# Kernel optimization log

Measured on AMD Instinct MI355X. Metric: run time of the kernel, lower is better.

Reference implementation:

```python
import jax, jax.numpy as jnp
import numpy as np

B, S, H, NH, NF = 128, 1024, 768, 8, 8
FUSED = 3 * H + NF  # 2312


def _lin(k, o, i):
    return jax.random.normal(k, (o, i), jnp.float32) * (1.0 / np.sqrt(i))


def setup_inputs() -> dict:
    key = jax.random.key(0)
    ks = jax.random.split(key, 20)
    last_hidden = jax.random.normal(ks[0], (B, S, H), jnp.float32)
    arousal_feats = jax.random.normal(ks[1], (B, NF), jnp.float32)
    sep1 = jax.random.randint(ks[2], (B,), 2, 800)
    sep2 = jnp.minimum(sep1 + jax.random.randint(ks[3], (B,), 2, 200), S - 1)
    return {
        "last_hidden": last_hidden,
        "arousal_feats": arousal_feats,
        "sep1": sep1,
        "sep2": sep2,
        "in_proj_w": _lin(ks[4], 3 * H, H),
        "in_proj_b": jnp.zeros((3 * H,), jnp.float32),
        "out_w": _lin(ks[5], H, H),
        "out_b": jnp.zeros((H,), jnp.float32),
        "ln_g": jnp.ones((NF,), jnp.float32),
        "ln_b": jnp.zeros((NF,), jnp.float32),
        "va_w1": _lin(ks[6], 512, FUSED),
        "va_b1": jnp.zeros((512,), jnp.float32),
        "va_w2": _lin(ks[7], 128, 512),
        "va_b2": jnp.zeros((128,), jnp.float32),
        "va_w3": _lin(ks[8], 2, 128),
        "va_b3": jnp.zeros((2,), jnp.float32),
        "pol_w": _lin(ks[9], 3, FUSED),
        "pol_b": jnp.zeros((3,), jnp.float32),
        "aro_w": _lin(ks[10], 3, FUSED),
        "aro_b": jnp.zeros((3,), jnp.float32),
    }


def reference(last_hidden, arousal_feats, sep1, sep2, in_proj_w, in_proj_b,
              out_w, out_b, ln_g, ln_b, va_w1, va_b1, va_w2, va_b2,
              va_w3, va_b3, pol_w, pol_b, aro_w, aro_b):
    b, s, h = last_hidden.shape
    nh, dh = NH, h // NH
    pos = jnp.arange(s)[None, :]  # [1,S]
    # ragged boundaries -> masks (honors s1>1 / s2>s1+1 fallbacks to CLS token)
    text_mask = jnp.where((sep1 > 1)[:, None], (pos >= 1) & (pos < sep1[:, None]), pos == 0)
    asp_mask = jnp.where((sep2 > sep1 + 1)[:, None], (pos > sep1[:, None]) & (pos < sep2[:, None]), pos == 0)
    amf = asp_mask.astype(last_hidden.dtype)
    asp_query = (last_hidden * amf[..., None]).sum(1) / amf.sum(1)[:, None]  # [B,H]
    # MultiheadAttention with a single query per sample, keys/values masked to text span
    wq, wk, wv = jnp.split(in_proj_w, 3, axis=0)
    bq, bk, bv = jnp.split(in_proj_b, 3)
    q = (asp_query @ wq.T + bq).reshape(b, nh, dh)
    k = (last_hidden @ wk.T + bk).reshape(b, s, nh, dh)
    v = (last_hidden @ wv.T + bv).reshape(b, s, nh, dh)
    scale = 1.0 / np.sqrt(dh)
    scores = jnp.einsum('bhd,bshd->bhs', q, k) * scale
    scores = jnp.where(text_mask[:, None, :], scores, -jnp.inf)
    attn = jax.nn.softmax(scores, axis=-1)
    ctx = jnp.einsum('bhs,bshd->bhd', attn, v).reshape(b, h)
    cross = ctx @ out_w.T + out_b  # [B,H]
    # ArousalFeatureNorm ~ LayerNorm over feature dim
    mu = arousal_feats.mean(-1, keepdims=True)
    var = arousal_feats.var(-1, keepdims=True)
    aro_n = (arousal_feats - mu) / jnp.sqrt(var + 1e-5) * ln_g + ln_b
    fused = jnp.concatenate([last_hidden[:, 0], cross, asp_query, aro_n], axis=-1)
    hdn = jax.nn.gelu(fused @ va_w1.T + va_b1, approximate=False)
    hdn = jax.nn.gelu(hdn @ va_w2.T + va_b2, approximate=False)
    va = hdn @ va_w3.T + va_b3
    pol = fused @ pol_w.T + pol_b
    aro = fused @ aro_w.T + aro_b
    return (va, pol, aro)
```

## Files before the change

kernel.cpp:

```cpp
#include <hip/hip_runtime.h>
#include <hip/hip_bf16.h>
#include <math.h>

#define B 128
#define S 1024
#define H 768
#define NH 8
#define DH 96
#define FUSED 2312
#define KCHUNK 128
#define NOUT 544
#define MD 800
#define NZ_NOCTX 13
#define NZ_CTX 5
#define NZTOT 18
#define ASL 8
#define NSL 16
#define FCH 16
#define SCALE 0.10206207261596575f
#define GELU_C 0.70710678118654752f

#define MTILES (17 * 25)
#define HTILES (NZ_NOCTX * 4 * 17)

__device__ __forceinline__ float dot4(float4 a, float4 b) {
    return a.x * b.x + a.y * b.y + a.z * b.z + a.w * b.w;
}
__device__ __forceinline__ float gelu(float x) {
    return 0.5f * x * (1.0f + erff(x * GELU_C));
}

__device__ __forceinline__ const float* wrow_sel(int n, const float* va_w1,
                                                 const float* pol_w,
                                                 const float* aro_w,
                                                 bool& valid) {
    valid = true;
    if (n < 512) return va_w1 + (size_t)n * FUSED;
    if (n < 515) return pol_w + (size_t)(n - 512) * FUSED;
    if (n < 518) return aro_w + (size_t)(n - 515) * FUSED;
    valid = false;
    return va_w1;
}

__global__ __launch_bounds__(256) void k1_aspq_m(
        const float* __restrict__ lh,
        const int* __restrict__ sep1,
        const int* __restrict__ sep2,
        const float* __restrict__ va_w1,
        const float* __restrict__ pol_w,
        const float* __restrict__ aro_w,
        const float* __restrict__ out_w,
        const float* __restrict__ out_b,
        float* __restrict__ aspp,
        float* __restrict__ Mbuf) {
    int bid = blockIdx.x, t = threadIdx.x;
    if (bid < B * ASL) {
        if (t >= 192) return;
        int b = bid >> 3, z = bid & 7;
        int s1 = sep1[b], s2 = sep2[b];
        int lo, hi;
        if (s2 > s1 + 1) { lo = s1 + 1; hi = s2; } else { lo = 0; hi = 1; }
        const float* base = lh + ((size_t)b * S) * H + 4 * t;
        float4 a = {0.f, 0.f, 0.f, 0.f};
        for (int s = lo + z; s < hi; s += ASL) {
            float4 r = *(const float4*)(base + (size_t)s * H);
            a.x += r.x; a.y += r.y; a.z += r.z; a.w += r.w;
        }
        *(float4*)(aspp + (size_t)z * (B * H) + b * H + 4 * t) = a;
        return;
    }
    int j = bid - B * ASL;
    int n0 = (j / 25) * 32, d0 = (j % 25) * 32;
    __shared__ float As[32][33];
    __shared__ float Ws[32][33];
    int tx = t & 31, ty = t >> 5;
    int lr = t >> 3, lc = (t & 7) * 4;
    float acc[4] = {0.f, 0.f, 0.f, 0.f};
    for (int k0 = 0; k0 < H; k0 += 32) {
        {
            int n = n0 + lr;
            bool valid;
            const float* wr = wrow_sel(n, va_w1, pol_w, aro_w, valid);
            float4 a = {0.f, 0.f, 0.f, 0.f};
            if (valid) a = *(const float4*)(wr + H + k0 + lc);
            As[lr][lc] = a.x; As[lr][lc + 1] = a.y;
            As[lr][lc + 2] = a.z; As[lr][lc + 3] = a.w;
        }
        {
            int c = k0 + lr;
            float4 w;
            if (d0 < H) {
                w = *(const float4*)(out_w + (size_t)c * H + d0 + lc);
            } else {
                w.x = (lc == 0) ? out_b[c] : 0.f;
                w.y = 0.f; w.z = 0.f; w.w = 0.f;
            }
            Ws[lc][lr] = w.x; Ws[lc + 1][lr] = w.y;
            Ws[lc + 2][lr] = w.z; Ws[lc + 3][lr] = w.w;
        }
        __syncthreads();
#pragma unroll
        for (int kk = 0; kk < 32; ++kk) {
            float wv = Ws[tx][kk];
#pragma unroll
            for (int i = 0; i < 4; ++i)
                acc[i] += As[ty + 8 * i][kk] * wv;
        }
        __syncthreads();
    }
#pragma unroll
    for (int i = 0; i < 4; ++i)
        Mbuf[(size_t)(n0 + ty + 8 * i) * MD + d0 + tx] = acc[i];
}

__global__ void qu_kernel(const float* __restrict__ aspp,
                          const int* __restrict__ sep1,
                          const int* __restrict__ sep2,
                          const float* __restrict__ wq,
                          const float* __restrict__ bq,
                          const float* __restrict__ wk,
                          float* __restrict__ aspq,
                          float* __restrict__ U) {
    int h = blockIdx.x, b = blockIdx.y, t = threadIdx.x;
    int s1 = sep1[b], s2 = sep2[b];
    int lo, hi;
    if (s2 > s1 + 1) { lo = s1 + 1; hi = s2; } else { lo = 0; hi = 1; }
    float inv = 1.0f / (float)(hi - lo);
    __shared__ float aq[H];
    __shared__ float qh[DH];
    for (int c = t; c < H; c += 256) {
        float a = 0.f;
#pragma unroll
        for (int z = 0; z < ASL; ++z)
            a += aspp[(size_t)z * (B * H) + b * H + c];
        a *= inv;
        aq[c] = a;
        if (h == 0) aspq[b * H + c] = a;
    }
    __syncthreads();
    int wave = t >> 6, lane = t & 63;
#pragma unroll
    for (int i = 0; i < 24; ++i) {
        int d = wave * 24 + i;
        const float* wrow = wq + (size_t)(h * DH + d) * H;
        float a = 0.f;
#pragma unroll
        for (int j = 0; j < H / 64; ++j) a += wrow[lane + 64 * j] * aq[lane + 64 * j];
        for (int off = 32; off; off >>= 1) a += __shfl_xor(a, off);
        if (lane == 0) qh[d] = a + bq[h * DH + d];
    }
    __syncthreads();
    if (t < 192) {
        float4 u = {0.f, 0.f, 0.f, 0.f};
        for (int d = 0; d < DH; ++d) {
            float qd = qh[d];
            float4 w = *(const float4*)(wk + (size_t)(h * DH + d) * H + 4 * t);
            u.x += qd * w.x; u.y += qd * w.y;
            u.z += qd * w.z; u.w += qd * w.w;
        }
        *(float4*)(U + ((size_t)b * NH + h) * H + 4 * t) = u;
    }
}

__global__ __launch_bounds__(512) void k3_flash_hdn1(
        const float* __restrict__ lhg,
        const float* __restrict__ U,
        const int* __restrict__ sep1,
        const float* __restrict__ aspq,
        const float* __restrict__ aro_f,
        const float* __restrict__ ln_g,
        const float* __restrict__ ln_b,
        const float* __restrict__ va_w1,
        const float* __restrict__ pol_w,
        const float* __restrict__ aro_w,
        float* __restrict__ Op,
        float* __restrict__ mlb,
        float* __restrict__ hdn1p) {
    __shared__ float smem[FCH * H];
    int bid = blockIdx.x, t = threadIdx.x;

    if (bid < B * NSL) {
        int b = bid >> 4, z = bid & 15;
        int wave = t >> 6, lane = t & 63;
        int s1 = sep1[b];
        int tlo = (s1 > 1) ? 1 : 0;
        int thi = (s1 > 1) ? s1 : 1;
        int span = thi - tlo;
        int nrows = (span > z) ? ((span - z - 1) / NSL + 1) : 0;
        float (*lhs)[H] = (float(*)[H])smem;

        const float4* Uh = (const float4*)(U + ((size_t)b * NH + wave) * H);
        float4 u0 = Uh[lane], u1 = Uh[lane + 64], u2 = Uh[lane + 128];
        float4 O0 = {0.f, 0.f, 0.f, 0.f}, O1 = O0, O2 = O0;
        float m = -1e30f, l = 0.f;
        int rid = t >> 5, cid = t & 31;

        for (int j0 = 0; j0 < nrows; j0 += FCH) {
            int nv = min(FCH, nrows - j0);
            if (rid < nv) {
                int sg = tlo + z + NSL * (j0 + rid);
                const float4* row = (const float4*)(lhg + ((size_t)b * S + sg) * H);
                float4* dst = (float4*)lhs[rid];
#pragma unroll
                for (int k = 0; k < 6; ++k) dst[cid + 32 * k] = row[cid + 32 * k];
            }
            __syncthreads();
            for (int r = 0; r < nv; ++r) {
                const float4* xr = (const float4*)lhs[r];
                float4 x0 = xr[lane], x1 = xr[lane + 64], x2 = xr[lane + 128];
                float s = dot4(u0, x0) + dot4(u1, x1) + dot4(u2, x2);
                for (int off = 32; off; off >>= 1) s += __shfl_xor(s, off);
                s *= SCALE;
                if (s <= m) {
                    float p = __expf(s - m);
                    l += p;
                    O0.x += p * x0.x; O0.y += p * x0.y; O0.z += p * x0.z; O0.w += p * x0.w;
                    O1.x += p * x1.x; O1.y += p * x1.y; O1.z += p * x1.z; O1.w += p * x1.w;
                    O2.x += p * x2.x; O2.y += p * x2.y; O2.z += p * x2.z; O2.w += p * x2.w;
                } else {
                    float c = __expf(m - s);
                    m = s;
                    l = l * c + 1.0f;
                    O0.x = O0.x * c + x0.x; O0.y = O0.y * c + x0.y;
                    O0.z = O0.z * c + x0.z; O0.w = O0.w * c + x0.w;
                    O1.x = O1.x * c + x1.x; O1.y = O1.y * c + x1.y;
                    O1.z = O1.z * c + x1.z; O1.w = O1.w * c + x1.w;
                    O2.x = O2.x * c + x2.x; O2.y = O2.y * c + x2.y;
                    O2.z = O2.z * c + x2.z; O2.w = O2.w * c + x2.w;
                }
            }
            __syncthreads();
        }
        float4* Ob = (float4*)(Op + (((size_t)z * B + b) * NH + wave) * H);
        Ob[lane] = O0; Ob[lane + 64] = O1; Ob[lane + 128] = O2;
        if (lane == 0) {
            float* ml = mlb + ((size_t)z * B + b) * NH * 2;
            ml[2 * wave]     = m;
            ml[2 * wave + 1] = l;
        }
        return;
    }

    int j = bid - B * NSL;
    int z13 = j / 68, rem = j % 68;
    int z = (z13 < 6) ? z13 : z13 + 6;
    int m0 = (rem / 17) * 32, n0 = (rem % 17) * 32;
    int kbase = z * KCHUNK;
    float (*As)[33] = (float(*)[33])smem;
    float (*Ws)[33] = (float(*)[33])(smem + 32 * 33);
    int tx = t & 31, ty = t >> 5;
    int lr = t >> 3, lc = (t & 7) * 4;
    float acc[4] = {0.f, 0.f, 0.f, 0.f};
    bool active = (t < 256);
    for (int k0 = kbase; k0 < kbase + KCHUNK; k0 += 32) {
        if (active) {
            int bb = m0 + lr;
            int k = k0 + lc;
            float4 a;
            if (k < 768) {
                a = *(const float4*)(lhg + (size_t)bb * S * H + k);
            } else if (k < 2304) {
                a = *(const float4*)(aspq + (size_t)bb * H + (k - 1536));
            } else if (k < FUSED) {
                const float* af = aro_f + bb * 8;
                float mu = 0.f;
#pragma unroll
                for (int jj = 0; jj < 8; ++jj) mu += af[jj];
                mu *= 0.125f;
                float var = 0.f;
#pragma unroll
                for (int jj = 0; jj < 8; ++jj) { float d = af[jj] - mu; var += d * d; }
                var *= 0.125f;
                float rs = rsqrtf(var + 1e-5f);
                int c = k - 2304;
                a.x = (af[c]     - mu) * rs * ln_g[c]     + ln_b[c];
                a.y = (af[c + 1] - mu) * rs * ln_g[c + 1] + ln_b[c + 1];
                a.z = (af[c + 2] - mu) * rs * ln_g[c + 2] + ln_b[c + 2];
                a.w = (af[c + 3] - mu) * rs * ln_g[c + 3] + ln_b[c + 3];
            } else {
                a = {0.f, 0.f, 0.f, 0.f};
            }
            As[lr][lc] = a.x; As[lr][lc + 1] = a.y;
            As[lr][lc + 2] = a.z; As[lr][lc + 3] = a.w;
            int n = n0 + lr;
            int kk = min(k0 + lc, FUSED - 4);
            bool valid;
            const float* wr = wrow_sel(n, va_w1, pol_w, aro_w, valid);
            float4 w = {0.f, 0.f, 0.f, 0.f};
            if (valid) w = *(const float4*)(wr + kk);
            Ws[lr][lc] = w.x; Ws[lr][lc + 1] = w.y;
            Ws[lr][lc + 2] = w.z; Ws[lr][lc + 3] = w.w;
        }
        __syncthreads();
        if (active) {
#pragma unroll
            for (int kk = 0; kk < 32; ++kk) {
                float wv = Ws[tx][kk];
#pragma unroll
                for (int i = 0; i < 4; ++i)
                    acc[i] += As[ty + 8 * i][kk] * wv;
            }
        }
        __syncthreads();
    }
    if (active) {
        int n = n0 + tx;
#pragma unroll
        for (int i = 0; i < 4; ++i) {
            int mm = m0 + ty + 8 * i;
            hdn1p[(size_t)z13 * (B * NOUT) + (size_t)mm * NOUT + n] = acc[i];
        }
    }
}

__global__ void mergectx_kernel(const float* __restrict__ Op,
                                const float* __restrict__ mlb,
                                const float* __restrict__ wv,
                                const float* __restrict__ bv,
                                float* __restrict__ ctx) {
    int h = blockIdx.x, b = blockIdx.y, t = threadIdx.x;
    float M = -1e30f;
#pragma unroll
    for (int z = 0; z < NSL; ++z)
        M = fmaxf(M, mlb[(((size_t)z * B + b) * NH + h) * 2]);
    float wz[NSL], L = 0.f;
#pragma unroll
    for (int z = 0; z < NSL; ++z) {
        const float* ml = mlb + (((size_t)z * B + b) * NH + h) * 2;
        float e = __expf(ml[0] - M);
        wz[z] = e;
        L += e * ml[1];
    }
    float Li = 1.0f / L;
    __shared__ float wsum[H];
    for (int c = t; c < H; c += 256) {
        float a = 0.f;
#pragma unroll
        for (int z = 0; z < NSL; ++z)
            a += wz[z] * Op[(((size_t)z * B + b) * NH + h) * H + c];
        wsum[c] = a * Li;
    }
    __syncthreads();
    int wave = t >> 6, lane = t & 63;
#pragma unroll
    for (int i = 0; i < 24; ++i) {
        int d = wave * 24 + i;
        const float* wrow = wv + (size_t)(h * DH + d) * H;
        float a = 0.f;
#pragma unroll
        for (int j = 0; j < H / 64; ++j) a += wrow[lane + 64 * j] * wsum[lane + 64 * j];
        for (int off = 32; off; off >>= 1) a += __shfl_xor(a, off);
        if (lane == 0) ctx[b * H + h * DH + d] = a + bv[h * DH + d];
    }
}

__global__ __launch_bounds__(256) void k5_hdn1ctx(
        const float* __restrict__ ctx,
        const float* __restrict__ Mbuf,
        float* __restrict__ hdn1p) {
    int z = blockIdx.z;
    int n0 = blockIdx.x * 32, m0 = blockIdx.y * 32;
    int kbase = z * 160;
    __shared__ float As[32][33];
    __shared__ float Ws[32][33];
    int t = threadIdx.x;
    int tx = t & 31, ty = t >> 5;
    int lr = t >> 3, lc = (t & 7) * 4;
    float acc[4] = {0.f, 0.f, 0.f, 0.f};
    for (int k0 = kbase; k0 < kbase + 160; k0 += 32) {
        {
            int bb = m0 + lr;
            int k = k0 + lc;
            float4 a;
            if (k < 768)      a = *(const float4*)(ctx + (size_t)bb * H + k);
            else if (k == 768) a = {1.f, 0.f, 0.f, 0.f};
            else              a = {0.f, 0.f, 0.f, 0.f};
            As[lr][lc] = a.x; As[lr][lc + 1] = a.y;
            As[lr][lc + 2] = a.z; As[lr][lc + 3] = a.w;
        }
        {
            float4 w = *(const float4*)(Mbuf + (size_t)(n0 + lr) * MD + k0 + lc);
            Ws[lr][lc] = w.x; Ws[lr][lc + 1] = w.y;
            Ws[lr][lc + 2] = w.z; Ws[lr][lc + 3] = w.w;
        }
        __syncthreads();
#pragma unroll
        for (int kk = 0; kk < 32; ++kk) {
            float wv = Ws[tx][kk];
#pragma unroll
            for (int i = 0; i < 4; ++i)
                acc[i] += As[ty + 8 * i][kk] * wv;
        }
        __syncthreads();
    }
    int n = n0 + tx;
#pragma unroll
    for (int i = 0; i < 4; ++i) {
        int mm = m0 + ty + 8 * i;
        hdn1p[(size_t)(NZ_NOCTX + z) * (B * NOUT) + (size_t)mm * NOUT + n] = acc[i];
    }
}

__global__ __launch_bounds__(512) void mlp2_kernel(
        const float* __restrict__ hdn1p,
        const float* __restrict__ va_b1,
        const float* __restrict__ va_w2,
        const float* __restrict__ va_b2,
        const float* __restrict__ va_w3,
        const float* __restrict__ va_b3,
        const float* __restrict__ pol_b,
        const float* __restrict__ aro_b,
        float* __restrict__ out) {
    int b = blockIdx.x, t = threadIdx.x;
    int wave = t >> 6, lane = t & 63;
    __shared__ float hsS[512];
    __shared__ float h2S[128];
    {
        float s = 0.f;
#pragma unroll
        for (int z = 0; z < NZTOT; ++z)
            s += hdn1p[(size_t)z * (B * NOUT) + (size_t)b * NOUT + t];
        hsS[t] = gelu(s + va_b1[t]);
    }
    if (t < 6) {
        float s = 0.f;
#pragma unroll
        for (int z = 0; z < NZTOT; ++z)
            s += hdn1p[(size_t)z * (B * NOUT) + (size_t)b * NOUT + 512 + t];
        if (t < 3) out[256 + b * 3 + t]       = s + pol_b[t];
        else       out[640 + b * 3 + (t - 3)] = s + aro_b[t - 3];
    }
    __syncthreads();
#pragma unroll
    for (int i = 0; i < 16; ++i) {
        int n = wave * 16 + i;
        float a = 0.f;
#pragma unroll
        for (int j = 0; j < 8; ++j) {
            int k = lane + 64 * j;
            a += hsS[k] * va_w2[(size_t)n * 512 + k];
        }
        for (int off = 32; off; off >>= 1) a += __shfl_xor(a, off);
        if (lane == 0) h2S[n] = gelu(a + va_b2[n]);
    }
    __syncthreads();
    if (wave < 2) {
        float a = h2S[lane] * va_w3[wave * 128 + lane]
                + h2S[lane + 64] * va_w3[wave * 128 + lane + 64];
        for (int off = 32; off; off >>= 1) a += __shfl_xor(a, off);
        if (lane == 0) out[b * 2 + wave] = a + va_b3[wave];
    }
}

extern "C" void kernel_launch(void* const* d_in, const int* in_sizes, int n_in,
                              void* d_out, int out_size, void* d_ws, size_t ws_size,
                              hipStream_t stream) {
    const float* lh    = (const float*)d_in[0];
    const float* aro_f = (const float*)d_in[1];
    const int*   sep1  = (const int*)d_in[2];
    const int*   sep2  = (const int*)d_in[3];
    const float* in_w  = (const float*)d_in[4];
    const float* in_b  = (const float*)d_in[5];
    const float* out_w = (const float*)d_in[6];
    const float* out_b = (const float*)d_in[7];
    const float* ln_g  = (const float*)d_in[8];
    const float* ln_b  = (const float*)d_in[9];
    const float* va_w1 = (const float*)d_in[10];
    const float* va_b1 = (const float*)d_in[11];
    const float* va_w2 = (const float*)d_in[12];
    const float* va_b2 = (const float*)d_in[13];
    const float* va_w3 = (const float*)d_in[14];
    const float* va_b3 = (const float*)d_in[15];
    const float* pol_w = (const float*)d_in[16];
    const float* pol_b = (const float*)d_in[17];
    const float* aro_w = (const float*)d_in[18];
    const float* aro_b = (const float*)d_in[19];
    float* out = (float*)d_out;

    float* ws = (float*)d_ws;
    float* aspp   = ws;
    float* aspq   = aspp + ASL * B * H;
    float* Ubuf   = aspq + B * H;
    float* Opb    = Ubuf + B * NH * H;
    float* mlbuf  = Opb + (size_t)NSL * B * NH * H;
    float* ctx    = mlbuf + NSL * B * NH * 2;
    float* Mbuf   = ctx + B * H;
    float* hdn1p  = Mbuf + NOUT * MD;

    const float* wq = in_w;
    const float* wk = in_w + H * H;
    const float* wv = in_w + 2 * H * H;
    const float* bq = in_b;
    const float* bv = in_b + 2 * H;

    k1_aspq_m<<<B * ASL + MTILES, 256, 0, stream>>>(
        lh, sep1, sep2, va_w1, pol_w, aro_w, out_w, out_b, aspp, Mbuf);
    qu_kernel<<<dim3(NH, B), 256, 0, stream>>>(aspp, sep1, sep2, wq, bq, wk,
                                               aspq, Ubuf);
    k3_flash_hdn1<<<B * NSL + HTILES, 512, 0, stream>>>(
        lh, Ubuf, sep1, aspq, aro_f, ln_g, ln_b,
        va_w1, pol_w, aro_w, Opb, mlbuf, hdn1p);
    mergectx_kernel<<<dim3(NH, B), 256, 0, stream>>>(Opb, mlbuf, wv, bv, ctx);
    k5_hdn1ctx<<<dim3(17, 4, NZ_CTX), 256, 0, stream>>>(ctx, Mbuf, hdn1p);
    mlp2_kernel<<<B, 512, 0, stream>>>(hdn1p, va_b1, va_w2, va_b2,
                                       va_w3, va_b3, pol_b, aro_b, out);
}
```

Before: 214.3 us.

## Fuse six kernel launches into one cooperative persistent kernel with grid syncs

```diff
diff --git a/kernel.cpp b/kernel.cpp
--- a/kernel.cpp
+++ b/kernel.cpp
@@ -1,6 +1,9 @@
 #include <hip/hip_runtime.h>
+#include <hip/hip_cooperative_groups.h>
 #include <hip/hip_bf16.h>
 #include <math.h>
+
+namespace cg = cooperative_groups;
 
 #define B 128
 #define S 1024
@@ -17,11 +20,16 @@
 #define ASL 8
 #define NSL 16
 #define FCH 16
+#define GRID 256
 #define SCALE 0.10206207261596575f
 #define GELU_C 0.70710678118654752f
 
-#define MTILES (17 * 25)
-#define HTILES (NZ_NOCTX * 4 * 17)
+#define AJOBS (B * ASL)
+#define MJOBS (17 * 25)
+#define H1JOBS (7 * 4 * 17)
+#define H3JOBS (6 * 4 * 17)
+#define P0JOBS (AJOBS + MJOBS + H1JOBS)
+#define P2JOBS (B * NSL + H3JOBS)
 
 __device__ __forceinline__ float dot4(float4 a, float4 b) {
     return a.x * b.x + a.y * b.y + a.z * b.z + a.w * b.w;
@@ -29,7 +37,6 @@
 __device__ __forceinline__ float gelu(float x) {
     return 0.5f * x * (1.0f + erff(x * GELU_C));
 }
-
 __device__ __forceinline__ const float* wrow_sel(int n, const float* va_w1,
                                                  const float* pol_w,
                                                  const float* aro_w,
@@ -41,6 +48,470 @@
     valid = false;
     return va_w1;
 }
+
+__global__ __launch_bounds__(512, 4) void mega_kernel(
+        const float* __restrict__ lh,
+        const float* __restrict__ aro_f,
+        const int* __restrict__ sep1,
+        const int* __restrict__ sep2,
+        const float* __restrict__ in_w,
+        const float* __restrict__ in_b,
+        const float* __restrict__ out_w,
+        const float* __restrict__ out_b,
+        const float* __restrict__ ln_g,
+        const float* __restrict__ ln_b,
+        const float* __restrict__ va_w1,
+        const float* __restrict__ va_b1,
+        const float* __restrict__ va_w2,
+        const float* __restrict__ va_b2,
+        const float* __restrict__ va_w3,
+        const float* __restrict__ va_b3,
+        const float* __restrict__ pol_w,
+        const float* __restrict__ pol_b,
+        const float* __restrict__ aro_w,
+        const float* __restrict__ aro_b,
+        float* __restrict__ ws,
+        float* __restrict__ out) {
+    cg::grid_group gridg = cg::this_grid();
+    __shared__ float smem[FCH * H];
+
+    float* aspp  = ws;
+    float* aspq  = aspp + ASL * B * H;
+    float* Ubuf  = aspq + B * H;
+    float* Opb   = Ubuf + B * NH * H;
+    float* mlbuf = Opb + (size_t)NSL * B * NH * H;
+    float* ctx   = mlbuf + NSL * B * NH * 2;
+    float* Mbuf  = ctx + B * H;
+    float* hdn1p = Mbuf + NOUT * MD;
+
+    const float* wq = in_w;
+    const float* wk = in_w + H * H;
+    const float* wv = in_w + 2 * H * H;
+    const float* bq = in_b;
+    const float* bv = in_b + 2 * H;
+
+    int t = threadIdx.x;
+    int wave = t >> 6, lane = t & 63;
+    int nblk = gridDim.x;
+
+    for (int j = blockIdx.x; j < P0JOBS; j += nblk) {
+        if (j < AJOBS) {
+            if (t < 192) {
+                int b = j >> 3, z = j & 7;
+                int s1 = sep1[b], s2 = sep2[b];
+                int lo, hi;
+                if (s2 > s1 + 1) { lo = s1 + 1; hi = s2; } else { lo = 0; hi = 1; }
+                const float* base = lh + ((size_t)b * S) * H + 4 * t;
+                float4 a = {0.f, 0.f, 0.f, 0.f};
+                for (int s = lo + z; s < hi; s += ASL) {
+                    float4 r = *(const float4*)(base + (size_t)s * H);
+                    a.x += r.x; a.y += r.y; a.z += r.z; a.w += r.w;
+                }
+                *(float4*)(aspp + (size_t)z * (B * H) + b * H + 4 * t) = a;
+            }
+            __syncthreads();
+            continue;
+        }
+        float (*As)[33] = (float(*)[33])smem;
+        float (*Ws)[33] = (float(*)[33])(smem + 32 * 33);
+        int tx = t & 31, ty = (t >> 5) & 7;
+        int lr = (t & 255) >> 3, lc = (t & 7) * 4;
+        bool active = (t < 256);
+        float acc[4] = {0.f, 0.f, 0.f, 0.f};
+        if (j < AJOBS + MJOBS) {
+            int jm = j - AJOBS;
+            int n0 = (jm / 25) * 32, d0 = (jm % 25) * 32;
+            for (int k0 = 0; k0 < H; k0 += 32) {
+                if (active) {
+                    int n = n0 + lr;
+                    bool valid;
+                    const float* wr = wrow_sel(n, va_w1, pol_w, aro_w, valid);
+                    float4 a = {0.f, 0.f, 0.f, 0.f};
+                    if (valid) a = *(const float4*)(wr + H + k0 + lc);
+                    As[lr][lc] = a.x; As[lr][lc + 1] = a.y;
+                    As[lr][lc + 2] = a.z; As[lr][lc + 3] = a.w;
+                    int c = k0 + lr;
+                    float4 w;
+                    if (d0 < H) {
+                        w = *(const float4*)(out_w + (size_t)c * H + d0 + lc);
+                    } else {
+                        w.x = (lc == 0) ? out_b[c] : 0.f;
+                        w.y = 0.f; w.z = 0.f; w.w = 0.f;
+                    }
+                    Ws[lc][lr] = w.x; Ws[lc + 1][lr] = w.y;
+                    Ws[lc + 2][lr] = w.z; Ws[lc + 3][lr] = w.w;
+                }
+                __syncthreads();
+                if (active) {
+#pragma unroll
+                    for (int kk = 0; kk < 32; ++kk) {
+                        float wv2 = Ws[tx][kk];
+#pragma unroll
+                        for (int i = 0; i < 4; ++i)
+                            acc[i] += As[ty + 8 * i][kk] * wv2;
+                    }
+                }
+                __syncthreads();
+            }
+            if (active) {
+#pragma unroll
+                for (int i = 0; i < 4; ++i)
+                    Mbuf[(size_t)(n0 + ty + 8 * i) * MD + d0 + tx] = acc[i];
+            }
+            continue;
+        }
+        int jh = j - AJOBS - MJOBS;
+        int z13 = jh / 68, rem = jh % 68;
+        int z    = (z13 < 6) ? z13 : 18;
+        int slot = (z13 < 6) ? z13 : 12;
+        int m0 = (rem / 17) * 32, n0 = (rem % 17) * 32;
+        int kbase = z * KCHUNK;
+        for (int k0 = kbase; k0 < kbase + KCHUNK; k0 += 32) {
+            if (active) {
+                int bb = m0 + lr;
+                int k = k0 + lc;
+                float4 a;
+                if (k < 768) {
+                    a = *(const float4*)(lh + (size_t)bb * S * H + k);
+                } else if (k < FUSED) {
+                    const float* af = aro_f + bb * 8;
+                    float mu = 0.f;
+#pragma unroll
+                    for (int jj = 0; jj < 8; ++jj) mu += af[jj];
+                    mu *= 0.125f;
+                    float var = 0.f;
+#pragma unroll
+                    for (int jj = 0; jj < 8; ++jj) { float d = af[jj] - mu; var += d * d; }
+                    var *= 0.125f;
+                    float rs = rsqrtf(var + 1e-5f);
+                    int c = k - 2304;
+                    a.x = (af[c]     - mu) * rs * ln_g[c]     + ln_b[c];
+                    a.y = (af[c + 1] - mu) * rs * ln_g[c + 1] + ln_b[c + 1];
+                    a.z = (af[c + 2] - mu) * rs * ln_g[c + 2] + ln_b[c + 2];
+                    a.w = (af[c + 3] - mu) * rs * ln_g[c + 3] + ln_b[c + 3];
+                } else {
+                    a = {0.f, 0.f, 0.f, 0.f};
+                }
+                As[lr][lc] = a.x; As[lr][lc + 1] = a.y;
+                As[lr][lc + 2] = a.z; As[lr][lc + 3] = a.w;
+                int n = n0 + lr;
+                int kk = min(k0 + lc, FUSED - 4);
+                bool valid;
+                const float* wr = wrow_sel(n, va_w1, pol_w, aro_w, valid);
+                float4 w = {0.f, 0.f, 0.f, 0.f};
+                if (valid) w = *(const float4*)(wr + kk);
+                Ws[lr][lc] = w.x; Ws[lr][lc + 1] = w.y;
+                Ws[lr][lc + 2] = w.z; Ws[lr][lc + 3] = w.w;
+            }
+            __syncthreads();
+            if (active) {
+#pragma unroll
+                for (int kk = 0; kk < 32; ++kk) {
+                    float wv2 = Ws[tx][kk];
+#pragma unroll
+                    for (int i = 0; i < 4; ++i)
+                        acc[i] += As[ty + 8 * i][kk] * wv2;
+                }
+            }
+            __syncthreads();
+        }
+        if (active) {
+            int n = n0 + tx;
+#pragma unroll
+            for (int i = 0; i < 4; ++i) {
+                int mm = m0 + ty + 8 * i;
+                hdn1p[(size_t)slot * (B * NOUT) + (size_t)mm * NOUT + n] = acc[i];
+            }
+        }
+    }
+    gridg.sync();
+
+    for (int j = blockIdx.x; j < B * NH; j += nblk) {
+        int b = j >> 3, h = j & 7;
+        float* aq = smem;
+        float* qh = smem + H;
+        int s1 = sep1[b], s2 = sep2[b];
+        int lo, hi;
+        if (s2 > s1 + 1) { lo = s1 + 1; hi = s2; } else { lo = 0; hi = 1; }
+        float inv = 1.0f / (float)(hi - lo);
+        for (int c = t; c < H; c += 512) {
+            float a = 0.f;
+#pragma unroll
+            for (int z = 0; z < ASL; ++z)
+                a += aspp[(size_t)z * (B * H) + b * H + c];
+            a *= inv;
+            aq[c] = a;
+            if (h == 0) aspq[b * H + c] = a;
+        }
+        __syncthreads();
+#pragma unroll
+        for (int i = 0; i < 12; ++i) {
+            int d = wave * 12 + i;
+            const float* wrow = wq + (size_t)(h * DH + d) * H;
+            float a = 0.f;
+#pragma unroll
+            for (int jj = 0; jj < H / 64; ++jj)
+                a += wrow[lane + 64 * jj] * aq[lane + 64 * jj];
+            for (int off = 32; off; off >>= 1) a += __shfl_xor(a, off);
+            if (lane == 0) qh[d] = a + bq[h * DH + d];
+        }
+        __syncthreads();
+        if (t < 192) {
+            float4 u = {0.f, 0.f, 0.f, 0.f};
+            for (int d = 0; d < DH; ++d) {
+                float qd = qh[d];
+                float4 w = *(const float4*)(wk + (size_t)(h * DH + d) * H + 4 * t);
+                u.x += qd * w.x; u.y += qd * w.y;
+                u.z += qd * w.z; u.w += qd * w.w;
+            }
+            *(float4*)(Ubuf + ((size_t)b * NH + h) * H + 4 * t) = u;
+        }
+        __syncthreads();
+    }
+    gridg.sync();
+
+    for (int j = blockIdx.x; j < P2JOBS; j += nblk) {
+        if (j < B * NSL) {
+            int b = j >> 4, z = j & 15;
+            int s1 = sep1[b];
+            int tlo = (s1 > 1) ? 1 : 0;
+            int thi = (s1 > 1) ? s1 : 1;
+            int span = thi - tlo;
+            int nrows = (span > z) ? ((span - z - 1) / NSL + 1) : 0;
+            float (*lhs)[H] = (float(*)[H])smem;
+
+            const float4* Uh = (const float4*)(Ubuf + ((size_t)b * NH + wave) * H);
+            float4 u0 = Uh[lane], u1 = Uh[lane + 64], u2 = Uh[lane + 128];
+            float4 O0 = {0.f, 0.f, 0.f, 0.f}, O1 = O0, O2 = O0;
+            float m = -1e30f, l = 0.f;
+            int rid = t >> 5, cid = t & 31;
+
+            for (int j0 = 0; j0 < nrows; j0 += FCH) {
+                int nv = min(FCH, nrows - j0);
+                if (rid < nv) {
+                    int sg = tlo + z + NSL * (j0 + rid);
+                    const float4* row = (const float4*)(lh + ((size_t)b * S + sg) * H);
+                    float4* dst = (float4*)lhs[rid];
+#pragma unroll
+                    for (int k = 0; k < 6; ++k) dst[cid + 32 * k] = row[cid + 32 * k];
+                }
+                __syncthreads();
+                for (int r = 0; r < nv; ++r) {
+                    const float4* xr = (const float4*)lhs[r];
+                    float4 x0 = xr[lane], x1 = xr[lane + 64], x2 = xr[lane + 128];
+                    float s = dot4(u0, x0) + dot4(u1, x1) + dot4(u2, x2);
+                    for (int off = 32; off; off >>= 1) s += __shfl_xor(s, off);
+                    s *= SCALE;
+                    if (s <= m) {
+                        float p = __expf(s - m);
+                        l += p;
+                        O0.x += p * x0.x; O0.y += p * x0.y; O0.z += p * x0.z; O0.w += p * x0.w;
+                        O1.x += p * x1.x; O1.y += p * x1.y; O1.z += p * x1.z; O1.w += p * x1.w;
+                        O2.x += p * x2.x; O2.y += p * x2.y; O2.z += p * x2.z; O2.w += p * x2.w;
+                    } else {
+                        float c = __expf(m - s);
+                        m = s;
+                        l = l * c + 1.0f;
+                        O0.x = O0.x * c + x0.x; O0.y = O0.y * c + x0.y;
+                        O0.z = O0.z * c + x0.z; O0.w = O0.w * c + x0.w;
+                        O1.x = O1.x * c + x1.x; O1.y = O1.y * c + x1.y;
+                        O1.z = O1.z * c + x1.z; O1.w = O1.w * c + x1.w;
+                        O2.x = O2.x * c + x2.x; O2.y = O2.y * c + x2.y;
+                        O2.z = O2.z * c + x2.z; O2.w = O2.w * c + x2.w;
+                    }
+                }
+                __syncthreads();
+            }
+            float4* Ob = (float4*)(Opb + (((size_t)z * B + b) * NH + wave) * H);
+            Ob[lane] = O0; Ob[lane + 64] = O1; Ob[lane + 128] = O2;
+            if (lane == 0) {
+                float* ml = mlbuf + ((size_t)z * B + b) * NH * 2;
+                ml[2 * wave]     = m;
+                ml[2 * wave + 1] = l;
+            }
+            __syncthreads();
+            continue;
+        }
+        int jh = j - B * NSL;
+        int zi = jh / 68, rem = jh % 68;
+        int z = zi + 12, slot = zi + 6;
+        int m0 = (rem / 17) * 32, n0 = (rem % 17) * 32;
+        int kbase = z * KCHUNK;
+        float (*As)[33] = (float(*)[33])smem;
+        float (*Ws)[33] = (float(*)[33])(smem + 32 * 33);
+        int tx = t & 31, ty = (t >> 5) & 7;
+        int lr = (t & 255) >> 3, lc = (t & 7) * 4;
+        float acc[4] = {0.f, 0.f, 0.f, 0.f};
+        bool active = (t < 256);
+        for (int k0 = kbase; k0 < kbase + KCHUNK; k0 += 32) {
+            if (active) {
+                int bb = m0 + lr;
+                int k = k0 + lc;
+                float4 a = *(const float4*)(aspq + (size_t)bb * H + (k - 1536));
+                As[lr][lc] = a.x; As[lr][lc + 1] = a.y;
+                As[lr][lc + 2] = a.z; As[lr][lc + 3] = a.w;
+                int n = n0 + lr;
+                bool valid;
+                const float* wr = wrow_sel(n, va_w1, pol_w, aro_w, valid);
+                float4 w = {0.f, 0.f, 0.f, 0.f};
+                if (valid) w = *(const float4*)(wr + k);
+                Ws[lr][lc] = w.x; Ws[lr][lc + 1] = w.y;
+                Ws[lr][lc + 2] = w.z; Ws[lr][lc + 3] = w.w;
+            }
+            __syncthreads();
+            if (active) {
+#pragma unroll
+                for (int kk = 0; kk < 32; ++kk) {
+                    float wv2 = Ws[tx][kk];
+#pragma unroll
+                    for (int i = 0; i < 4; ++i)
+                        acc[i] += As[ty + 8 * i][kk] * wv2;
+                }
+            }
+            __syncthreads();
+        }
+        if (active) {
+            int n = n0 + tx;
+#pragma unroll
+            for (int i = 0; i < 4; ++i) {
+                int mm = m0 + ty + 8 * i;
+                hdn1p[(size_t)slot * (B * NOUT) + (size_t)mm * NOUT + n] = acc[i];
+            }
+        }
+    }
+    gridg.sync();
+
+    for (int j = blockIdx.x; j < B * NH; j += nblk) {
+        int b = j >> 3, h = j & 7;
+        float* wsum = smem;
+        float M = -1e30f;
+#pragma unroll
+        for (int z = 0; z < NSL; ++z)
+            M = fmaxf(M, mlbuf[(((size_t)z * B + b) * NH + h) * 2]);
+        float wz[NSL], L = 0.f;
+#pragma unroll
+        for (int z = 0; z < NSL; ++z) {
+            const float* ml = mlbuf + (((size_t)z * B + b) * NH + h) * 2;
+            float e = __expf(ml[0] - M);
+            wz[z] = e;
+            L += e * ml[1];
+        }
+        float Li = 1.0f / L;
+        for (int c = t; c < H; c += 512) {
+            float a = 0.f;
+#pragma unroll
+            for (int z = 0; z < NSL; ++z)
+                a += wz[z] * Opb[(((size_t)z * B + b) * NH + h) * H + c];
+            wsum[c] = a * Li;
+        }
+        __syncthreads();
+#pragma unroll
+        for (int i = 0; i < 12; ++i) {
+            int d = wave * 12 + i;
+            const float* wrow = wv + (size_t)(h * DH + d) * H;
+            float a = 0.f;
+#pragma unroll
+            for (int jj = 0; jj < H / 64; ++jj)
+                a += wrow[lane + 64 * jj] * wsum[lane + 64 * jj];
+            for (int off = 32; off; off >>= 1) a += __shfl_xor(a, off);
+            if (lane == 0) ctx[b * H + h * DH + d] = a + bv[h * DH + d];
+        }
+        __syncthreads();
+    }
+    gridg.sync();
+
+    for (int j = blockIdx.x; j < 17 * 4 * NZ_CTX; j += nblk) {
+        int z = j / 68, rem = j % 68;
+        int m0 = (rem / 17) * 32, n0 = (rem % 17) * 32;
+        int kbase = z * 160;
+        float (*As)[33] = (float(*)[33])smem;
+        float (*Ws)[33] = (float(*)[33])(smem + 32 * 33);
+        int tx = t & 31, ty = (t >> 5) & 7;
+        int lr = (t & 255) >> 3, lc = (t & 7) * 4;
+        float acc[4] = {0.f, 0.f, 0.f, 0.f};
+        bool active = (t < 256);
+        for (int k0 = kbase; k0 < kbase + 160; k0 += 32) {
+            if (active) {
+                int bb = m0 + lr;
+                int k = k0 + lc;
+                float4 a;
+                if (k < 768)       a = *(const float4*)(ctx + (size_t)bb * H + k);
+                else if (k == 768) a = {1.f, 0.f, 0.f, 0.f};
+                else               a = {0.f, 0.f, 0.f, 0.f};
+                As[lr][lc] = a.x; As[lr][lc + 1] = a.y;
+                As[lr][lc + 2] = a.z; As[lr][lc + 3] = a.w;
+                float4 w = *(const float4*)(Mbuf + (size_t)(n0 + lr) * MD + k0 + lc);
+                Ws[lr][lc] = w.x; Ws[lr][lc + 1] = w.y;
+                Ws[lr][lc + 2] = w.z; Ws[lr][lc + 3] = w.w;
+            }
+            __syncthreads();
+            if (active) {
+#pragma unroll
+                for (int kk = 0; kk < 32; ++kk) {
+                    float wv2 = Ws[tx][kk];
+#pragma unroll
+                    for (int i = 0; i < 4; ++i)
+                        acc[i] += As[ty + 8 * i][kk] * wv2;
+                }
+            }
+            __syncthreads();
+        }
+        if (active) {
+            int n = n0 + tx;
+#pragma unroll
+            for (int i = 0; i < 4; ++i) {
+                int mm = m0 + ty + 8 * i;
+                hdn1p[(size_t)(NZ_NOCTX + z) * (B * NOUT) + (size_t)mm * NOUT + n] = acc[i];
+            }
+        }
+    }
+    gridg.sync();
+
+    for (int j = blockIdx.x; j < B; j += nblk) {
+        int b = j;
+        float* hsS = smem;
+        float* h2S = smem + 512;
+        {
+            float s = 0.f;
+#pragma unroll
+            for (int z = 0; z < NZTOT; ++z)
+                s += hdn1p[(size_t)z * (B * NOUT) + (size_t)b * NOUT + t];
+            hsS[t] = gelu(s + va_b1[t]);
+        }
+        if (t < 6) {
+            float s = 0.f;
+#pragma unroll
+            for (int z = 0; z < NZTOT; ++z)
+                s += hdn1p[(size_t)z * (B * NOUT) + (size_t)b * NOUT + 512 + t];
+            if (t < 3) out[256 + b * 3 + t]       = s + pol_b[t];
+            else       out[640 + b * 3 + (t - 3)] = s + aro_b[t - 3];
+        }
+        __syncthreads();
+#pragma unroll
+        for (int i = 0; i < 16; ++i) {
+            int n = wave * 16 + i;
+            float a = 0.f;
+#pragma unroll
+            for (int jj = 0; jj < 8; ++jj) {
+                int k = lane + 64 * jj;
+                a += hsS[k] * va_w2[(size_t)n * 512 + k];
+            }
+            for (int off = 32; off; off >>= 1) a += __shfl_xor(a, off);
+            if (lane == 0) h2S[n] = gelu(a + va_b2[n]);
+        }
+        __syncthreads();
+        if (wave < 2) {
+            float a = h2S[lane] * va_w3[wave * 128 + lane]
+                    + h2S[lane + 64] * va_w3[wave * 128 + lane + 64];
+            for (int off = 32; off; off >>= 1) a += __shfl_xor(a, off);
+            if (lane == 0) out[b * 2 + wave] = a + va_b3[wave];
+        }
+        __syncthreads();
+    }
+}
+
+#define MTILES (17 * 25)
+#define HTILES (NZ_NOCTX * 4 * 17)
 
 __global__ __launch_bounds__(256) void k1_aspq_m(
         const float* __restrict__ lh,
@@ -372,9 +843,9 @@
             int bb = m0 + lr;
             int k = k0 + lc;
             float4 a;
-            if (k < 768)      a = *(const float4*)(ctx + (size_t)bb * H + k);
+            if (k < 768)       a = *(const float4*)(ctx + (size_t)bb * H + k);
             else if (k == 768) a = {1.f, 0.f, 0.f, 0.f};
-            else              a = {0.f, 0.f, 0.f, 0.f};
+            else               a = {0.f, 0.f, 0.f, 0.f};
             As[lr][lc] = a.x; As[lr][lc + 1] = a.y;
             As[lr][lc + 2] = a.z; As[lr][lc + 3] = a.w;
         }
@@ -475,17 +946,29 @@
     const float* pol_b = (const float*)d_in[17];
     const float* aro_w = (const float*)d_in[18];
     const float* aro_b = (const float*)d_in[19];
-    float* out = (float*)d_out;
-
-    float* ws = (float*)d_ws;
-    float* aspp   = ws;
-    float* aspq   = aspp + ASL * B * H;
-    float* Ubuf   = aspq + B * H;
-    float* Opb    = Ubuf + B * NH * H;
-    float* mlbuf  = Opb + (size_t)NSL * B * NH * H;
-    float* ctx    = mlbuf + NSL * B * NH * 2;
-    float* Mbuf   = ctx + B * H;
-    float* hdn1p  = Mbuf + NOUT * MD;
+    float* wsf = (float*)d_ws;
+    float* outp = (float*)d_out;
+
+    void* params[] = {
+        (void*)&lh, (void*)&aro_f, (void*)&sep1, (void*)&sep2,
+        (void*)&in_w, (void*)&in_b, (void*)&out_w, (void*)&out_b,
+        (void*)&ln_g, (void*)&ln_b, (void*)&va_w1, (void*)&va_b1,
+        (void*)&va_w2, (void*)&va_b2, (void*)&va_w3, (void*)&va_b3,
+        (void*)&pol_w, (void*)&pol_b, (void*)&aro_w, (void*)&aro_b,
+        (void*)&wsf, (void*)&outp};
+    hipError_t err = hipLaunchCooperativeKernel(
+        (const void*)mega_kernel, dim3(GRID), dim3(512), params, 0, stream);
+    if (err == hipSuccess) return;
+    (void)hipGetLastError();
+
+    float* aspp  = wsf;
+    float* aspq  = aspp + ASL * B * H;
+    float* Ubuf  = aspq + B * H;
+    float* Opb   = Ubuf + B * NH * H;
+    float* mlbuf = Opb + (size_t)NSL * B * NH * H;
+    float* ctx   = mlbuf + NSL * B * NH * 2;
+    float* Mbuf  = ctx + B * H;
+    float* hdn1p = Mbuf + NOUT * MD;
 
     const float* wq = in_w;
     const float* wk = in_w + H * H;
@@ -503,5 +986,5 @@
     mergectx_kernel<<<dim3(NH, B), 256, 0, stream>>>(Opb, mlbuf, wv, bv, ctx);
     k5_hdn1ctx<<<dim3(17, 4, NZ_CTX), 256, 0, stream>>>(ctx, Mbuf, hdn1p);
     mlp2_kernel<<<B, 512, 0, stream>>>(hdn1p, va_b1, va_w2, va_b2,
-                                       va_w3, va_b3, pol_b, aro_b, out);
-}
+                                       va_w3, va_b3, pol_b, aro_b, outp);
+}
```

New measurement: 585.8 us. +173.3%, slower.
